# Optimization experiments

Measured on AMD Instinct MI355X. Metric: run time of the kernel, lower is better.

Reference implementation:

```python
import jax, jax.numpy as jnp
import numpy as np

N_NODES = 50000
N_EDGES = 800000
D_FEAT = 128
EMBED = 128
HEADS = 8
HEAD_DIM = EMBED // HEADS


def setup_inputs() -> dict:
    key = jax.random.key(0)
    ks = jax.random.split(key, 10)
    xavier = jax.nn.initializers.xavier_normal()
    return {
        "nodes": jax.random.normal(ks[0], (N_NODES, D_FEAT), jnp.float32),
        "edges": jax.random.normal(ks[1], (N_EDGES, D_FEAT), jnp.float32),
        "senders": jax.random.randint(ks[2], (N_EDGES,), 0, N_NODES, jnp.int32),
        "receivers": jax.random.randint(ks[3], (N_EDGES,), 0, N_NODES, jnp.int32),
        "Ws_k": xavier(ks[4], (D_FEAT, EMBED), jnp.float32),
        "Ws_b": jnp.zeros((EMBED,), jnp.float32),
        "Wr_k": xavier(ks[5], (D_FEAT, EMBED), jnp.float32),
        "Wr_b": jnp.zeros((EMBED,), jnp.float32),
        "We_k": xavier(ks[6], (D_FEAT, EMBED), jnp.float32),
        "We_b": jnp.zeros((EMBED,), jnp.float32),
        "a": xavier(ks[7], (HEADS, HEAD_DIM), jnp.float32),
    }


def reference(nodes, edges, senders, receivers, Ws_k, Ws_b, Wr_k, Wr_b, We_k, We_b, a):
    N = nodes.shape[0]
    E = edges.shape[0]
    H, D = a.shape
    # Node-level projections (linear, so equivalent to projecting gathered edge endpoints)
    hs = nodes @ Ws_k + Ws_b            # [N, HD]  (W_s on sent attributes)
    hr = nodes @ Wr_k + Wr_b            # [N, HD]  (W_r on received attributes)
    he = edges @ We_k + We_b            # [E, HD]  (W_e on edge attributes)
    sent = hs[senders]                  # [E, HD]
    x = jax.nn.leaky_relu(sent + hr[receivers] + he)  # default slope 0.01, as original
    xh = x.reshape(E, H, D)
    logits = jnp.sum(xh * a, axis=-1)   # [E, H]
    # segment_softmax over receivers (stable: subtract per-segment max)
    mx = jax.ops.segment_max(logits, receivers, num_segments=N)  # [N, H]
    mx = jnp.where(jnp.isfinite(mx), mx, 0.0)
    ex = jnp.exp(logits - mx[receivers])                         # [E, H]
    denom = jax.ops.segment_sum(ex, receivers, num_segments=N)   # [N, H]
    w = ex / denom[receivers]                                    # [E, H]
    msg = (w[..., None] * sent.reshape(E, H, D)).reshape(E, H * D)
    out = jax.ops.segment_sum(msg, receivers, num_segments=N)    # [N, HD]
    return out
```

## Files before the change

### kernel.cpp

```cpp
#include <hip/hip_runtime.h>

#define N_NODES 50000
#define N_EDGES 800000
#define D 128
#define HEADS 8

typedef __attribute__((ext_vector_type(8))) short short8b;
typedef __attribute__((ext_vector_type(4))) float f32x4;

__device__ __forceinline__ unsigned short f2bf_rne(float f) {
    unsigned int u = __float_as_uint(f);
    u += 0x7FFFu + ((u >> 16) & 1u);
    return (unsigned short)(u >> 16);
}
__device__ __forceinline__ float bf2f(unsigned short u) {
    return __uint_as_float(((unsigned int)u) << 16);
}

#define K1_ROWS 256
__global__ __launch_bounds__(256, 3) void k_node_proj_mfma(
    const float* __restrict__ nodes,
    const float* __restrict__ Ws, const float* __restrict__ bs,
    const float* __restrict__ Wr, const float* __restrict__ br,
    unsigned short* __restrict__ hsb, unsigned short* __restrict__ hrb)
{
    __shared__ __align__(16) unsigned short WT[D][136];
    __shared__ __align__(16) unsigned short At[64][136];
    const int ntiles = (N_NODES + K1_ROWS - 1) / K1_ROWS;
    int bx = blockIdx.x;
    int proj = (bx >= ntiles) ? 1 : 0;
    int tile = proj ? (bx - ntiles) : bx;
    const float* W    = proj ? Wr : Ws;
    const float* bias = proj ? br : bs;
    unsigned short* outp = proj ? hrb : hsb;
    int t = threadIdx.x;
    int lane = t & 63;
    int wv = t >> 6;
    int lg = lane >> 4;
    int li = lane & 15;

    #pragma unroll 8
    for (int j = 0; j < 64; ++j) {
        int idx = t + 256 * j;
        int k = idx >> 7, c = idx & 127;
        WT[c][k] = f2bf_rne(W[idx]);
    }
    float b_ct[8];
    #pragma unroll
    for (int ct = 0; ct < 8; ++ct) b_ct[ct] = bias[ct * 16 + li];

    #pragma unroll 1
    for (int sub = 0; sub < 4; ++sub) {
        int row0 = tile * K1_ROWS + sub * 64;
        if (row0 >= N_NODES) break;
        __syncthreads();
        {
            const float4* Nv = (const float4*)nodes;
            #pragma unroll
            for (int j = 0; j < 8; ++j) {
                int fi = t + 256 * j;
                int r = row0 + (fi >> 5);
                float4 v = make_float4(0.f, 0.f, 0.f, 0.f);
                if (r < N_NODES) v = Nv[(size_t)r * 32 + (fi & 31)];
                ushort4 b;
                b.x = f2bf_rne(v.x); b.y = f2bf_rne(v.y);
                b.z = f2bf_rne(v.z); b.w = f2bf_rne(v.w);
                *(ushort4*)&At[fi >> 5][(fi & 31) * 4] = b;
            }
        }
        __syncthreads();

        short8b afr[4];
        #pragma unroll
        for (int kb = 0; kb < 4; ++kb)
            afr[kb] = *(const short8b*)&At[wv * 16 + li][kb * 32 + lg * 8];

        #pragma unroll
        for (int ct = 0; ct < 8; ++ct) {
            f32x4 acc = {0.f, 0.f, 0.f, 0.f};
            #pragma unroll
            for (int kb = 0; kb < 4; ++kb) {
                short8b bfr = *(const short8b*)&WT[ct * 16 + li][kb * 32 + lg * 8];
                acc = __builtin_amdgcn_mfma_f32_16x16x32_bf16(afr[kb], bfr, acc, 0, 0, 0);
            }
            #pragma unroll
            for (int j = 0; j < 4; ++j) {
                int r = row0 + wv * 16 + lg * 4 + j;
                if (r < N_NODES)
                    outp[(size_t)r * D + ct * 16 + li] = f2bf_rne(acc[j] + b_ct[ct]);
            }
        }
    }
}

__global__ __launch_bounds__(256) void k_hist(
    const int* __restrict__ receivers, int* __restrict__ deg)
{
    int i = blockIdx.x * 256 + threadIdx.x;
    if (i < N_EDGES) atomicAdd(&deg[receivers[i]], 1);
}

#define SCAN_CHUNK 49
__global__ __launch_bounds__(1024) void k_scan(
    const int* __restrict__ deg, int* __restrict__ rowptr, int* __restrict__ cursor)
{
    __shared__ int sm[1024];
    int t = threadIdx.x;
    int base = t * SCAN_CHUNK;
    int lsum = 0;
    #pragma unroll 4
    for (int i = 0; i < SCAN_CHUNK; ++i) {
        int idx = base + i;
        if (idx < N_NODES) lsum += deg[idx];
    }
    sm[t] = lsum;
    __syncthreads();
    for (int off = 1; off < 1024; off <<= 1) {
        int v = (t >= off) ? sm[t - off] : 0;
        __syncthreads();
        sm[t] += v;
        __syncthreads();
    }
    int run = (t > 0) ? sm[t - 1] : 0;
    for (int i = 0; i < SCAN_CHUNK; ++i) {
        int idx = base + i;
        if (idx < N_NODES) {
            rowptr[idx] = run;
            cursor[idx] = run;
            run += deg[idx];
        }
    }
    if (t == 1023) rowptr[N_NODES] = sm[1023];
}

__global__ __launch_bounds__(256) void k_fill(
    const int* __restrict__ receivers, const int* __restrict__ senders,
    int* __restrict__ cursor,
    int* __restrict__ eids, int* __restrict__ s_csr, int* __restrict__ r_csr)
{
    int i = blockIdx.x * 256 + threadIdx.x;
    if (i < N_EDGES) {
        int r = receivers[i];
        int pos = atomicAdd(&cursor[r], 1);
        eids[pos]  = i;
        s_csr[pos] = senders[i];
        r_csr[pos] = r;
    }
}

#define BLK_E 64
__global__ __launch_bounds__(256, 3) void k_edge_logits_mfma(
    const float* __restrict__ edges,
    const int* __restrict__ eids, const int* __restrict__ s_csr,
    const int* __restrict__ r_csr,
    const float* __restrict__ We, const float* __restrict__ be,
    const float* __restrict__ a,
    const unsigned short* __restrict__ hsb, const unsigned short* __restrict__ hrb,
    float* __restrict__ ex)
{
    __shared__ __align__(16) unsigned short WeT[D][136];
    __shared__ __align__(16) unsigned short Et[BLK_E][136];
    int t = threadIdx.x;
    int lane = t & 63;
    int wv = t >> 6;
    int lg = lane >> 4;
    int li = lane & 15;

    #pragma unroll 8
    for (int j = 0; j < 64; ++j) {
        int idx = t + 256 * j;
        int k = idx >> 7, c = idx & 127;
        WeT[c][k] = f2bf_rne(We[idx]);
    }
    float a_h[HEADS], be_h[HEADS];
    #pragma unroll
    for (int h = 0; h < HEADS; ++h) {
        a_h[h]  = a[h * 16 + li];
        be_h[h] = be[h * 16 + li];
    }
    int jm = li & 3;
    __syncthreads();

    const int ntiles = N_EDGES / BLK_E;
    for (int tile = blockIdx.x; tile < ntiles; tile += gridDim.x) {
        int pbase = tile * BLK_E + wv * 16;

        {
            const float4* Ev = (const float4*)edges;
            #pragma unroll
            for (int j = 0; j < 8; ++j) {
                int fi = lane + 64 * j;
                int rloc = fi >> 5;
                int e = eids[pbase + rloc];
                float4 v = Ev[(size_t)e * 32 + (fi & 31)];
                ushort4 b;
                b.x = f2bf_rne(v.x); b.y = f2bf_rne(v.y);
                b.z = f2bf_rne(v.z); b.w = f2bf_rne(v.w);
                *(ushort4*)&Et[wv * 16 + rloc][(fi & 31) * 4] = b;
            }
        }

        int sj[4], rj[4];
        #pragma unroll
        for (int j = 0; j < 4; ++j) {
            sj[j] = s_csr[pbase + lg * 4 + j];
            rj[j] = r_csr[pbase + lg * 4 + j];
        }
        unsigned short g_hs[4][HEADS], g_hr[4][HEADS];
        #pragma unroll
        for (int j = 0; j < 4; ++j) {
            const unsigned short* hsrow = hsb + (size_t)sj[j] * D + li;
            const unsigned short* hrrow = hrb + (size_t)rj[j] * D + li;
            #pragma unroll
            for (int h = 0; h < HEADS; ++h) {
                g_hs[j][h] = hsrow[h * 16];
                g_hr[j][h] = hrrow[h * 16];
            }
        }

        asm volatile("s_waitcnt lgkmcnt(0)" ::: "memory");
        __builtin_amdgcn_sched_barrier(0);

        short8b afr[4];
        #pragma unroll
        for (int kb = 0; kb < 4; ++kb)
            afr[kb] = *(const short8b*)&Et[wv * 16 + li][kb * 32 + lg * 8];

        #pragma unroll
        for (int h = 0; h < HEADS; ++h) {
            f32x4 acc = {0.f, 0.f, 0.f, 0.f};
            #pragma unroll
            for (int kb = 0; kb < 4; ++kb) {
                short8b bfr = *(const short8b*)&WeT[h * 16 + li][kb * 32 + lg * 8];
                acc = __builtin_amdgcn_mfma_f32_16x16x32_bf16(afr[kb], bfr, acc, 0, 0, 0);
            }
            float p[4];
            #pragma unroll
            for (int j = 0; j < 4; ++j) {
                float x = acc[j] + be_h[h] + bf2f(g_hs[j][h]) + bf2f(g_hr[j][h]);
                x = x > 0.f ? x : 0.01f * x;
                p[j] = x * a_h[h];
            }
            #pragma unroll
            for (int j = 0; j < 4; ++j) {
                p[j] += __shfl_xor(p[j], 1);
                p[j] += __shfl_xor(p[j], 2);
            }
            float q = (jm & 1) ? ((jm & 2) ? p[3] : p[1])
                               : ((jm & 2) ? p[2] : p[0]);
            q += __shfl_xor(q, 4);
            q += __shfl_xor(q, 8);
            float e_ = __expf(q);
            if (li < 4) {
                int pos = pbase + lg * 4 + li;
                ex[(size_t)pos * HEADS + h] = e_;
            }
        }
        __builtin_amdgcn_wave_barrier();
    }
}

__global__ __launch_bounds__(256) void k_gather_out(
    const int* __restrict__ rowptr, const int* __restrict__ s_csr,
    const unsigned short* __restrict__ hsb, const float* __restrict__ ex,
    float* __restrict__ out)
{
    int r = blockIdx.x * 4 + (threadIdx.x >> 6);
    int l = threadIdx.x & 63;
    int h = l >> 3;
    int beg = rowptr[r], end = rowptr[r + 1];

    float2 acc = make_float2(0.f, 0.f);
    float dsum = 0.f;
    for (int j0 = beg; j0 < end; j0 += 16) {
        int cnt = end - j0;
        int s[16]; float w[16];
        #pragma unroll
        for (int q = 0; q < 16; ++q)
            if (q < cnt) { s[q] = s_csr[j0 + q]; w[q] = ex[(size_t)(j0 + q) * HEADS + h]; }
        #pragma unroll
        for (int q = 0; q < 16; ++q)
            if (q < cnt) {
                ushort2 hv = *(const ushort2*)&hsb[(size_t)s[q] * D + 2 * l];
                acc.x += w[q] * bf2f(hv.x);
                acc.y += w[q] * bf2f(hv.y);
                dsum  += w[q];
            }
    }
    float inv = (end > beg && dsum != 0.f) ? (1.0f / dsum) : 0.f;
    acc.x *= inv; acc.y *= inv;
    *(float2*)&out[(size_t)r * D + 2 * l] = acc;
}

extern "C" void kernel_launch(void* const* d_in, const int* in_sizes, int n_in,
                              void* d_out, int out_size, void* d_ws, size_t ws_size,
                              hipStream_t stream) {
    const float* nodes     = (const float*)d_in[0];
    const float* edges     = (const float*)d_in[1];
    const int*   senders   = (const int*)d_in[2];
    const int*   receivers = (const int*)d_in[3];
    const float* Ws = (const float*)d_in[4];
    const float* bs = (const float*)d_in[5];
    const float* Wr = (const float*)d_in[6];
    const float* br = (const float*)d_in[7];
    const float* We = (const float*)d_in[8];
    const float* be = (const float*)d_in[9];
    const float* a  = (const float*)d_in[10];
    float* out = (float*)d_out;

    unsigned short* hsb = (unsigned short*)d_ws;
    unsigned short* hrb = hsb + (size_t)N_NODES * D;
    float* ex   = (float*)(hrb + (size_t)N_NODES * D);
    int* deg    = (int*)(ex + (size_t)N_EDGES * HEADS);
    int* rowptr = deg + N_NODES;
    int* cursor = rowptr + N_NODES + 1;
    int* eids   = cursor + N_NODES;
    int* s_csr  = eids + N_EDGES;
    int* r_csr  = s_csr + N_EDGES;

    hipMemsetAsync(deg, 0, N_NODES * sizeof(int), stream);
    k_hist<<<N_EDGES / 256, 256, 0, stream>>>(receivers, deg);
    k_scan<<<1, 1024, 0, stream>>>(deg, rowptr, cursor);
    k_fill<<<N_EDGES / 256, 256, 0, stream>>>(receivers, senders, cursor,
                                              eids, s_csr, r_csr);
    int ntiles_n = (N_NODES + K1_ROWS - 1) / K1_ROWS;
    k_node_proj_mfma<<<ntiles_n * 2, 256, 0, stream>>>(nodes, Ws, bs, Wr, br, hsb, hrb);
    k_edge_logits_mfma<<<2048, 256, 0, stream>>>(edges, eids, s_csr, r_csr,
                                                 We, be, a, hsb, hrb, ex);
    k_gather_out<<<N_NODES / 4, 256, 0, stream>>>(rowptr, s_csr, hsb, ex, out);
}
```

Measured before the change: 462.5 us.

## Interleave bf16 node projections by head lane for vectorized 16-byte access

```diff
diff --git a/kernel.cpp b/kernel.cpp
--- a/kernel.cpp
+++ b/kernel.cpp
@@ -6,6 +6,7 @@
 #define HEADS 8
 
 typedef __attribute__((ext_vector_type(8))) short short8b;
+typedef __attribute__((ext_vector_type(8))) unsigned short ushort8v;
 typedef __attribute__((ext_vector_type(4))) float f32x4;
 
 __device__ __forceinline__ unsigned short f2bf_rne(float f) {
@@ -75,6 +76,7 @@
         for (int kb = 0; kb < 4; ++kb)
             afr[kb] = *(const short8b*)&At[wv * 16 + li][kb * 32 + lg * 8];
 
+        f32x4 accs[8];
         #pragma unroll
         for (int ct = 0; ct < 8; ++ct) {
             f32x4 acc = {0.f, 0.f, 0.f, 0.f};
@@ -83,11 +85,22 @@
                 short8b bfr = *(const short8b*)&WT[ct * 16 + li][kb * 32 + lg * 8];
                 acc = __builtin_amdgcn_mfma_f32_16x16x32_bf16(afr[kb], bfr, acc, 0, 0, 0);
             }
-            #pragma unroll
-            for (int j = 0; j < 4; ++j) {
-                int r = row0 + wv * 16 + lg * 4 + j;
-                if (r < N_NODES)
-                    outp[(size_t)r * D + ct * 16 + li] = f2bf_rne(acc[j] + b_ct[ct]);
+            accs[ct] = acc;
+        }
+        #pragma unroll
+        for (int j = 0; j < 4; ++j) {
+            int r = row0 + wv * 16 + lg * 4 + j;
+            if (r < N_NODES) {
+                uint4 w;
+                w.x = (unsigned)f2bf_rne(accs[0][j] + b_ct[0])
+                    | ((unsigned)f2bf_rne(accs[1][j] + b_ct[1]) << 16);
+                w.y = (unsigned)f2bf_rne(accs[2][j] + b_ct[2])
+                    | ((unsigned)f2bf_rne(accs[3][j] + b_ct[3]) << 16);
+                w.z = (unsigned)f2bf_rne(accs[4][j] + b_ct[4])
+                    | ((unsigned)f2bf_rne(accs[5][j] + b_ct[5]) << 16);
+                w.w = (unsigned)f2bf_rne(accs[6][j] + b_ct[6])
+                    | ((unsigned)f2bf_rne(accs[7][j] + b_ct[7]) << 16);
+                *(uint4*)&outp[(size_t)r * D + li * 8] = w;
             }
         }
     }
@@ -206,16 +219,11 @@
             sj[j] = s_csr[pbase + lg * 4 + j];
             rj[j] = r_csr[pbase + lg * 4 + j];
         }
-        unsigned short g_hs[4][HEADS], g_hr[4][HEADS];
+        ushort8v g_hs[4], g_hr[4];
         #pragma unroll
         for (int j = 0; j < 4; ++j) {
-            const unsigned short* hsrow = hsb + (size_t)sj[j] * D + li;
-            const unsigned short* hrrow = hrb + (size_t)rj[j] * D + li;
-            #pragma unroll
-            for (int h = 0; h < HEADS; ++h) {
-                g_hs[j][h] = hsrow[h * 16];
-                g_hr[j][h] = hrrow[h * 16];
-            }
+            g_hs[j] = *(const ushort8v*)(hsb + (size_t)sj[j] * D + li * 8);
+            g_hr[j] = *(const ushort8v*)(hrb + (size_t)rj[j] * D + li * 8);
         }
 
         asm volatile("s_waitcnt lgkmcnt(0)" ::: "memory");
@@ -267,29 +275,35 @@
 {
     int r = blockIdx.x * 4 + (threadIdx.x >> 6);
     int l = threadIdx.x & 63;
-    int h = l >> 3;
+    int h1 = 2 * (l & 3);
+    int c1 = (l >> 2) + 16 * h1;
     int beg = rowptr[r], end = rowptr[r + 1];
 
     float2 acc = make_float2(0.f, 0.f);
-    float dsum = 0.f;
+    float ds1 = 0.f, ds2 = 0.f;
     for (int j0 = beg; j0 < end; j0 += 16) {
         int cnt = end - j0;
-        int s[16]; float w[16];
+        int s[16]; float2 w2[16];
         #pragma unroll
         for (int q = 0; q < 16; ++q)
-            if (q < cnt) { s[q] = s_csr[j0 + q]; w[q] = ex[(size_t)(j0 + q) * HEADS + h]; }
+            if (q < cnt) {
+                s[q]  = s_csr[j0 + q];
+                w2[q] = *(const float2*)&ex[(size_t)(j0 + q) * HEADS + h1];
+            }
         #pragma unroll
         for (int q = 0; q < 16; ++q)
             if (q < cnt) {
                 ushort2 hv = *(const ushort2*)&hsb[(size_t)s[q] * D + 2 * l];
-                acc.x += w[q] * bf2f(hv.x);
-                acc.y += w[q] * bf2f(hv.y);
-                dsum  += w[q];
-            }
-    }
-    float inv = (end > beg && dsum != 0.f) ? (1.0f / dsum) : 0.f;
-    acc.x *= inv; acc.y *= inv;
-    *(float2*)&out[(size_t)r * D + 2 * l] = acc;
+                acc.x += w2[q].x * bf2f(hv.x);
+                acc.y += w2[q].y * bf2f(hv.y);
+                ds1   += w2[q].x;
+                ds2   += w2[q].y;
+            }
+    }
+    float i1 = (end > beg && ds1 != 0.f) ? (1.0f / ds1) : 0.f;
+    float i2 = (end > beg && ds2 != 0.f) ? (1.0f / ds2) : 0.f;
+    out[(size_t)r * D + c1]      = acc.x * i1;
+    out[(size_t)r * D + c1 + 16] = acc.y * i2;
 }
 
 extern "C" void kernel_launch(void* const* d_in, const int* in_sizes, int n_in,
```

New measurement: 484.3 us. 1.05x slower.

## Pack CSR edge records into int4 and enlarge edge-logit blocks

Applied to the files above, without the earlier changes.

```diff
diff --git a/kernel.cpp b/kernel.cpp
--- a/kernel.cpp
+++ b/kernel.cpp
@@ -135,24 +135,20 @@
 
 __global__ __launch_bounds__(256) void k_fill(
     const int* __restrict__ receivers, const int* __restrict__ senders,
-    int* __restrict__ cursor,
-    int* __restrict__ eids, int* __restrict__ s_csr, int* __restrict__ r_csr)
+    int* __restrict__ cursor, int4* __restrict__ csr4)
 {
     int i = blockIdx.x * 256 + threadIdx.x;
     if (i < N_EDGES) {
         int r = receivers[i];
         int pos = atomicAdd(&cursor[r], 1);
-        eids[pos]  = i;
-        s_csr[pos] = senders[i];
-        r_csr[pos] = r;
-    }
-}
-
-#define BLK_E 64
-__global__ __launch_bounds__(256, 3) void k_edge_logits_mfma(
+        csr4[pos] = make_int4(i, senders[i], r, 0);
+    }
+}
+
+#define BLK_E 128
+__global__ __launch_bounds__(512, 4) void k_edge_logits_mfma(
     const float* __restrict__ edges,
-    const int* __restrict__ eids, const int* __restrict__ s_csr,
-    const int* __restrict__ r_csr,
+    const int4* __restrict__ csr4,
     const float* __restrict__ We, const float* __restrict__ be,
     const float* __restrict__ a,
     const unsigned short* __restrict__ hsb, const unsigned short* __restrict__ hrb,
@@ -166,9 +162,9 @@
     int lg = lane >> 4;
     int li = lane & 15;
 
-    #pragma unroll 8
-    for (int j = 0; j < 64; ++j) {
-        int idx = t + 256 * j;
+    #pragma unroll 4
+    for (int j = 0; j < 32; ++j) {
+        int idx = t + 512 * j;
         int k = idx >> 7, c = idx & 127;
         WeT[c][k] = f2bf_rne(We[idx]);
     }
@@ -182,29 +178,29 @@
     __syncthreads();
 
     const int ntiles = N_EDGES / BLK_E;
+    const float4* Ev = (const float4*)edges;
+
     for (int tile = blockIdx.x; tile < ntiles; tile += gridDim.x) {
         int pbase = tile * BLK_E + wv * 16;
 
-        {
-            const float4* Ev = (const float4*)edges;
-            #pragma unroll
-            for (int j = 0; j < 8; ++j) {
-                int fi = lane + 64 * j;
-                int rloc = fi >> 5;
-                int e = eids[pbase + rloc];
-                float4 v = Ev[(size_t)e * 32 + (fi & 31)];
-                ushort4 b;
-                b.x = f2bf_rne(v.x); b.y = f2bf_rne(v.y);
-                b.z = f2bf_rne(v.z); b.w = f2bf_rne(v.w);
-                *(ushort4*)&Et[wv * 16 + rloc][(fi & 31) * 4] = b;
-            }
+        #pragma unroll
+        for (int j = 0; j < 8; ++j) {
+            int fi = lane + 64 * j;
+            int rloc = fi >> 5;
+            int e = csr4[pbase + rloc].x;
+            float4 v = Ev[(size_t)e * 32 + (fi & 31)];
+            ushort4 b;
+            b.x = f2bf_rne(v.x); b.y = f2bf_rne(v.y);
+            b.z = f2bf_rne(v.z); b.w = f2bf_rne(v.w);
+            *(ushort4*)&Et[wv * 16 + rloc][(fi & 31) * 4] = b;
         }
 
         int sj[4], rj[4];
         #pragma unroll
         for (int j = 0; j < 4; ++j) {
-            sj[j] = s_csr[pbase + lg * 4 + j];
-            rj[j] = r_csr[pbase + lg * 4 + j];
+            int4 rec = csr4[pbase + lg * 4 + j];
+            sj[j] = rec.y;
+            rj[j] = rec.z;
         }
         unsigned short g_hs[4][HEADS], g_hr[4][HEADS];
         #pragma unroll
@@ -261,7 +257,7 @@
 }
 
 __global__ __launch_bounds__(256) void k_gather_out(
-    const int* __restrict__ rowptr, const int* __restrict__ s_csr,
+    const int* __restrict__ rowptr, const int4* __restrict__ csr4,
     const unsigned short* __restrict__ hsb, const float* __restrict__ ex,
     float* __restrict__ out)
 {
@@ -277,7 +273,7 @@
         int s[16]; float w[16];
         #pragma unroll
         for (int q = 0; q < 16; ++q)
-            if (q < cnt) { s[q] = s_csr[j0 + q]; w[q] = ex[(size_t)(j0 + q) * HEADS + h]; }
+            if (q < cnt) { s[q] = csr4[j0 + q].y; w[q] = ex[(size_t)(j0 + q) * HEADS + h]; }
         #pragma unroll
         for (int q = 0; q < 16; ++q)
             if (q < cnt) {
@@ -314,18 +310,17 @@
     int* deg    = (int*)(ex + (size_t)N_EDGES * HEADS);
     int* rowptr = deg + N_NODES;
     int* cursor = rowptr + N_NODES + 1;
-    int* eids   = cursor + N_NODES;
-    int* s_csr  = eids + N_EDGES;
-    int* r_csr  = s_csr + N_EDGES;
-
-    hipMemsetAsync(deg, 0, N_NODES * sizeof(int), stream);
+    size_t off = (size_t)(cursor + N_NODES - (int*)d_ws);
+    off = (off + 3) & ~(size_t)3;
+    int4* csr4 = (int4*)((int*)d_ws + off);
+
+    (void)hipMemsetAsync(deg, 0, N_NODES * sizeof(int), stream);
     k_hist<<<N_EDGES / 256, 256, 0, stream>>>(receivers, deg);
     k_scan<<<1, 1024, 0, stream>>>(deg, rowptr, cursor);
-    k_fill<<<N_EDGES / 256, 256, 0, stream>>>(receivers, senders, cursor,
-                                              eids, s_csr, r_csr);
+    k_fill<<<N_EDGES / 256, 256, 0, stream>>>(receivers, senders, cursor, csr4);
     int ntiles_n = (N_NODES + K1_ROWS - 1) / K1_ROWS;
     k_node_proj_mfma<<<ntiles_n * 2, 256, 0, stream>>>(nodes, Ws, bs, Wr, br, hsb, hrb);
-    k_edge_logits_mfma<<<2048, 256, 0, stream>>>(edges, eids, s_csr, r_csr,
-                                                 We, be, a, hsb, hrb, ex);
-    k_gather_out<<<N_NODES / 4, 256, 0, stream>>>(rowptr, s_csr, hsb, ex, out);
-}
+    k_edge_logits_mfma<<<512, 512, 0, stream>>>(edges, csr4, We, be, a,
+                                                hsb, hrb, ex);
+    k_gather_out<<<N_NODES / 4, 256, 0, stream>>>(rowptr, csr4, hsb, ex, out);
+}
```

After: 505.1 us. 1.09x slower.
